# Optimization experiments

Measured on AMD Instinct MI355X. Metric: run time of the kernel, lower is better.

## Reference

```python
import jax, jax.numpy as jnp
import numpy as np

HEAD_NUM = 16
NEG_BIG = -2.0**32 + 1.0


def _pos_encoding(T, D):
    pos = np.arange(T)[:, None].astype(np.float64)
    i = np.arange(D)[None, :].astype(np.float64)
    angle = pos / np.power(10000.0, 2.0 * i / D)
    pe = np.empty((T, D), dtype=np.float64)
    pe[:, 0::2] = np.sin(angle[:, 0::2])
    pe[:, 1::2] = np.cos(angle[:, 1::2])
    return jnp.asarray(pe * (D ** 0.5), dtype=jnp.float32)  # scale=True


def setup_inputs() -> dict:
    key = jax.random.key(0)
    ks = jax.random.split(key, 9)
    B, T, D = 32, 512, 1024
    return {
        "queries": jax.random.normal(ks[0], (B, T, D), jnp.float32),
        "keys": jax.random.normal(ks[1], (B, T, D), jnp.float32),
        "query_masks": jax.random.randint(ks[2], (B, 1), 1, T + 1, jnp.int32),
        "key_masks": jax.random.randint(ks[3], (B, 1), 1, T + 1, jnp.int32),
        "W_Query": jax.random.normal(ks[4], (D, D), jnp.float32) * 0.02,
        "W_key": jax.random.normal(ks[5], (D, D), jnp.float32) * 0.02,
        "W_Value": jax.random.normal(ks[6], (D, D), jnp.float32) * 0.02,
        "fw1": jax.random.normal(ks[7], (D, 4 * D), jnp.float32) * 0.02,
        "fw2": jax.random.normal(ks[8], (4 * D, D), jnp.float32) * 0.02,
    }


def reference(queries, keys, query_masks, key_masks, W_Query, W_key, W_Value, fw1, fw2):
    B, T, D = queries.shape
    h = HEAD_NUM
    d = D // h
    pe = _pos_encoding(T, D)  # [T, D]

    # faithful to source: queries get PE; keys = PE(queries_with_PE) (keys input unused)
    q_pe = queries + pe[None]
    k_pe = q_pe + pe[None]

    qs = jnp.einsum('btd,de->bte', q_pe, W_Query)
    ks_ = jnp.einsum('btd,de->bte', k_pe, W_key)
    vs = jnp.einsum('btd,de->bte', ks_, W_Value)  # faithful: values from projected keys

    def split_heads(x):  # [B,T,h*d] -> [h,B,T,d] (matches tf.split/concat on axis 0)
        return x.reshape(B, T, h, d).transpose(2, 0, 1, 3)

    q4, k4, v4 = split_heads(qs), split_heads(ks_), split_heads(vs)

    scores = jnp.einsum('hbqd,hbkd->hbqk', q4, k4) / (d ** 0.5)

    pos = jnp.arange(T)
    km = (pos[None, :] < key_masks).astype(jnp.float32)    # [B,T]
    qm = (pos[None, :] < query_masks).astype(jnp.float32)  # [B,T]

    scores = jnp.where(km[None, :, None, :] == 1.0, scores, NEG_BIG)
    scores = scores - jnp.max(scores, axis=-1, keepdims=True)
    attn = jax.nn.softmax(scores, axis=-1)
    attn = attn * qm[None, :, :, None]

    out = jnp.einsum('hbqk,hbkd->hbqd', attn, v4)
    result = out.transpose(1, 2, 0, 3).reshape(B, T, D)  # merge heads (head-major)

    result = result + q_pe  # use_res
    # feed forward (use_layer_norm=False, no dropout at inference)
    hmid = jax.nn.relu(jnp.einsum('btd,df->btf', result, fw1))
    result = result + jnp.einsum('btf,fd->btd', hmid, fw2)

    # output_type == 'mean'
    return jnp.mean(result, axis=1, keepdims=True)  # [B,1,D]
```

## Files before the change

kernel.cpp:

```cpp
#include <hip/hip_runtime.h>

constexpr int B_  = 32;
constexpr int T_  = 512;
constexpr int D_  = 1024;
constexpr int NH_ = 16;
constexpr int DH_ = 64;
constexpr int F_  = 4096;
constexpr int BT_ = B_ * T_;

typedef __attribute__((ext_vector_type(8))) short bf16x8;
typedef __attribute__((ext_vector_type(4))) float f32x4;

#define DEVI __device__ __forceinline__

DEVI unsigned short f2bf(float f) {
  union { float f; unsigned u; } uf; uf.f = f;
  unsigned r = uf.u + 0x7fffu + ((uf.u >> 16) & 1u);
  return (unsigned short)(r >> 16);
}
DEVI float b2f(unsigned short h) {
  union { unsigned u; float f; } uf; uf.u = ((unsigned)h) << 16;
  return uf.f;
}
DEVI void gload16(const void* g, void* l) {
  __builtin_amdgcn_global_load_lds(
      (const __attribute__((address_space(1))) void*)(uintptr_t)g,
      (__attribute__((address_space(3))) void*)(unsigned)(uintptr_t)l, 16, 0, 0);
}

__global__ void pe_kernel(float* __restrict__ pe) {
  int idx = blockIdx.x * 256 + threadIdx.x;
  int t = idx >> 10, j = idx & 1023;
  float inv = exp2f(-(2.0f * (float)j / 1024.0f) * 13.2877123795494f);
  float ang = (float)t * inv;
  float v = (j & 1) ? cosf(ang) : sinf(ang);
  pe[idx] = v * 32.0f;
}

__global__ void pack_kernel(const float* __restrict__ q, const float* __restrict__ pe,
                            unsigned short* __restrict__ q_pe, unsigned short* __restrict__ k_pe) {
  long i = ((long)blockIdx.x * 256 + threadIdx.x) * 4;
  const float4 qv = *(const float4*)(q + i);
  const float4 pv = *(const float4*)(pe + (i & (long)(T_ * D_ - 1)));
  ushort4 a, b;
  a.x = f2bf(qv.x + pv.x); a.y = f2bf(qv.y + pv.y);
  a.z = f2bf(qv.z + pv.z); a.w = f2bf(qv.w + pv.w);
  b.x = f2bf(qv.x + 2.f * pv.x); b.y = f2bf(qv.y + 2.f * pv.y);
  b.z = f2bf(qv.z + 2.f * pv.z); b.w = f2bf(qv.w + 2.f * pv.w);
  *(ushort4*)(q_pe + i) = a;
  *(ushort4*)(k_pe + i) = b;
}

__global__ void transpose_w(const float* __restrict__ W, unsigned short* __restrict__ Wt,
                            int K, int N) {
  __shared__ float tile[32][33];
  int tx = threadIdx.x & 31, ty = threadIdx.x >> 5;
  int bx = blockIdx.x, by = blockIdx.y;
  for (int i = 0; i < 4; i++) {
    int r = by * 32 + ty + i * 8;
    tile[ty + i * 8][tx] = W[(long)r * N + bx * 32 + tx];
  }
  __syncthreads();
  for (int i = 0; i < 4; i++) {
    int r = bx * 32 + ty + i * 8;
    Wt[(long)r * K + by * 32 + tx] = f2bf(tile[tx][ty + i * 8]);
  }
}

__global__ void cast_bf16(const float* __restrict__ W, unsigned short* __restrict__ Wb) {
  long i = ((long)blockIdx.x * 256 + threadIdx.x) * 4;
  const float4 v = *(const float4*)(W + i);
  ushort4 o;
  o.x = f2bf(v.x); o.y = f2bf(v.y); o.z = f2bf(v.z); o.w = f2bf(v.w);
  *(ushort4*)(Wb + i) = o;
}

__global__ void transpose_v(const unsigned short* __restrict__ vs, unsigned short* __restrict__ vt) {
  __shared__ unsigned short tile[64][65];
  int bh = blockIdx.y;
  int t0 = blockIdx.x * 64;
  int b = bh >> 4, h = bh & 15;
  int tx = threadIdx.x & 63, ty = threadIdx.x >> 6;
  for (int i = 0; i < 16; i++) {
    int r = i * 4 + ty;
    tile[r][tx] = vs[(long)(b * T_ + t0 + r) * D_ + h * DH_ + tx];
  }
  __syncthreads();
  for (int i = 0; i < 16; i++) {
    int j = i * 4 + ty;
    vt[((long)bh * DH_ + j) * T_ + t0 + tx] = tile[tx][j];
  }
}

template <int EPI>
__global__ __launch_bounds__(256) void gemm_bt(
    const unsigned short* __restrict__ A0, const unsigned short* __restrict__ Bt0,
    unsigned short* __restrict__ C0, float* __restrict__ hacc, int M, int N, int K) {
  __shared__ unsigned short As[128 * 32];
  __shared__ unsigned short Bs[128 * 32];
  const unsigned short* A  = A0;
  const unsigned short* Bt = Bt0;
  unsigned short* C        = C0;

  const int tid = threadIdx.x;
  const int lane = tid & 63, w = tid >> 6;
  const int wr = w >> 1, wc = w & 1;
  const int l15 = lane & 15, lhi = lane >> 4;
  const int brow = blockIdx.y * 128, bcol = blockIdx.x * 128;

  f32x4 acc[4][4] = {};
  const int o = tid * 16;
  const int srow = o >> 6;
  const int skel = (o & 63) >> 1;

  for (int kk = 0; kk < K; kk += 32) {
    gload16(A + (long)(brow + srow) * K + kk + skel,        (char*)As + o);
    gload16(A + (long)(brow + srow + 64) * K + kk + skel,   (char*)As + o + 4096);
    gload16(Bt + (long)(bcol + srow) * K + kk + skel,       (char*)Bs + o);
    gload16(Bt + (long)(bcol + srow + 64) * K + kk + skel,  (char*)Bs + o + 4096);
    __syncthreads();
    bf16x8 af[4], bfr[4];
    for (int m = 0; m < 4; m++)
      af[m] = *(const bf16x8*)((const char*)As + ((wr * 64 + m * 16 + l15) * 64 + lhi * 16));
    for (int n = 0; n < 4; n++)
      bfr[n] = *(const bf16x8*)((const char*)Bs + ((wc * 64 + n * 16 + l15) * 64 + lhi * 16));
    for (int m = 0; m < 4; m++)
      for (int n = 0; n < 4; n++)
        acc[m][n] = __builtin_amdgcn_mfma_f32_16x16x32_bf16(af[m], bfr[n], acc[m][n], 0, 0, 0);
    __syncthreads();
  }

  for (int m = 0; m < 4; m++)
    for (int n = 0; n < 4; n++) {
      int row = brow + wr * 64 + m * 16 + lhi * 4;
      int col = bcol + wc * 64 + n * 16 + l15;
      for (int r = 0; r < 4; r++)
        C[(long)(row + r) * N + col] = f2bf(acc[m][n][r]);
    }
}

template <int EPI>
__global__ __launch_bounds__(512, 2) void gemm8(
    const unsigned short* __restrict__ A0, const unsigned short* __restrict__ Bt0, unsigned short* __restrict__ C0,
    const unsigned short* __restrict__ A1, const unsigned short* __restrict__ Bt1, unsigned short* __restrict__ C1,
    const unsigned short* __restrict__ A2, const unsigned short* __restrict__ Bt2, unsigned short* __restrict__ C2,
    float* __restrict__ hacc, int N,
    const int* __restrict__ L0, const int* __restrict__ L1, const int* __restrict__ L2) {
  constexpr int K = 1024, NK = 16, NI = 8;
  __shared__ char lds[2][2][32768];

  const int z = blockIdx.z;
  const unsigned short* A  = (z == 0) ? A0  : (z == 1 ? A1  : A2);
  const unsigned short* Bt = (z == 0) ? Bt0 : (z == 1 ? Bt1 : Bt2);
  unsigned short* C        = (z == 0) ? C0  : (z == 1 ? C1  : C2);
  const int* L             = (z == 0) ? L0  : (z == 1 ? L1  : L2);

  const long brow = (long)blockIdx.x * 256, bcol = (long)blockIdx.y * 256;
  if (L && (brow & 256) && L[brow >> 9] <= 256) return;

  const int tid = threadIdx.x;
  const int lane = tid & 63, w = tid >> 6;
  const int wm = w >> 2, wn = w & 3;
  const int l15 = lane & 15, lhi = lane >> 4;

  const int drow = (tid * 16) >> 7;
  const int dcol = ((tid * 16) & 127) ^ ((drow & 7) << 4);
  const int sw   = (l15 & 7) << 4;

  f32x4 acc[8][4] = {};
  bf16x8 bfr[4][2], af[2][2];

  auto STAGE = [&](const unsigned short* __restrict__ P, long tb, int kt, int h, int buf, int op) {
    const unsigned short* g = P + (tb + h * 128 + drow) * (long)K + kt * 64 + (dcol >> 1);
    char* l = &lds[buf][op][h * 16384 + tid * 16];
    gload16(g, l);
    gload16(g + 64L * K, l + 8192);
  };
  auto LDA = [&](int buf, int q) {
#pragma unroll
    for (int mi = 0; mi < 2; mi++) {
      int row = wm * 128 + (q * 2 + mi) * 16 + l15;
#pragma unroll
      for (int kk = 0; kk < 2; kk++)
        af[mi][kk] = *(const bf16x8*)(&lds[buf][0][0] + (row << 7) + ((kk * 64 + lhi * 16) ^ sw));
    }
  };
  auto LDB = [&](int buf) {
#pragma unroll
    for (int n = 0; n < 4; n++) {
      int row = wn * 64 + n * 16 + l15;
#pragma unroll
      for (int kk = 0; kk < 2; kk++)
        bfr[n][kk] = *(const bf16x8*)(&lds[buf][1][0] + (row << 7) + ((kk * 64 + lhi * 16) ^ sw));
    }
  };
  auto MFMAQ = [&](int q) {
    __builtin_amdgcn_s_setprio(1);
#pragma unroll
    for (int mi = 0; mi < 2; mi++)
#pragma unroll
      for (int n = 0; n < 4; n++)
#pragma unroll
        for (int kk = 0; kk < 2; kk++)
          acc[q * 2 + mi][n] =
              __builtin_amdgcn_mfma_f32_16x16x32_bf16(af[mi][kk], bfr[n][kk], acc[q * 2 + mi][n], 0, 0, 0);
    __builtin_amdgcn_s_setprio(0);
  };
#define BAR() __builtin_amdgcn_s_barrier()
#define GATE4() asm volatile("s_waitcnt vmcnt(4)" ::: "memory")

  STAGE(A, brow, 0, 0, 0, 0);  STAGE(A, brow, 0, 1, 0, 0);
  STAGE(Bt, bcol, 0, 0, 0, 1); STAGE(Bt, bcol, 0, 1, 0, 1);
  STAGE(Bt, bcol, 1, 0, 1, 1); STAGE(Bt, bcol, 1, 1, 1, 1);
  GATE4();
  BAR();

  for (int i = 0; i < NI; ++i) {
    const int k1 = 2 * i + 1;
    const int ka = (2 * i + 2) & (NK - 1);
    const int kb = (2 * i + 3) & (NK - 1);
    LDA(0, 0); LDB(0); STAGE(A, brow, k1, 0, 1, 0);
    BAR(); MFMAQ(0); BAR();
    LDA(0, 1);         STAGE(A, brow, k1, 1, 1, 0);
    BAR(); MFMAQ(1); BAR();
    LDA(0, 2);         STAGE(Bt, bcol, ka, 0, 0, 1);
    BAR(); MFMAQ(2); BAR();
    LDA(0, 3);         STAGE(Bt, bcol, ka, 1, 0, 1);
    BAR(); MFMAQ(3);
    GATE4();
    BAR();
    LDA(1, 0); LDB(1); STAGE(A, brow, ka, 0, 0, 0);
    BAR(); MFMAQ(0); BAR();
    LDA(1, 1);         STAGE(A, brow, ka, 1, 0, 0);
    BAR(); MFMAQ(1); BAR();
    LDA(1, 2);         STAGE(Bt, bcol, kb, 0, 1, 1);
    BAR(); MFMAQ(2); BAR();
    LDA(1, 3);         STAGE(Bt, bcol, kb, 1, 1, 1);
    BAR(); MFMAQ(3);
    GATE4();
    BAR();
  }
#undef BAR
#undef GATE4

  if (EPI == 0) {
#pragma unroll
    for (int m = 0; m < 8; m++)
#pragma unroll
      for (int n = 0; n < 4; n++) {
        long row = brow + wm * 128 + m * 16 + lhi * 4;
        long col = bcol + wn * 64 + n * 16 + l15;
#pragma unroll
        for (int r = 0; r < 4; r++)
          C[(row + r) * (long)N + col] = f2bf(acc[m][n][r]);
      }
  } else {
    const int batch = (int)(brow >> 9);
#pragma unroll
    for (int n = 0; n < 4; n++) {
      float t = 0.f;
#pragma unroll
      for (int m = 0; m < 8; m++)
#pragma unroll
        for (int r = 0; r < 4; r++) t += fmaxf(acc[m][n][r], 0.f);
      t += __shfl_xor(t, 16);
      t += __shfl_xor(t, 32);
      if (lane < 16)
        atomicAdd(hacc + (long)batch * F_ + bcol + wn * 64 + n * 16 + l15, t);
    }
  }
}

__global__ __launch_bounds__(256, 3) void attn_kernel(
    const unsigned short* __restrict__ qs, const unsigned short* __restrict__ ks,
    const unsigned short* __restrict__ vt, const unsigned short* __restrict__ q_pe,
    const int* __restrict__ qmask, const int* __restrict__ kmask,
    unsigned short* __restrict__ res, float* __restrict__ racc) {
  __shared__ unsigned short Ks[2][64 * 64];
  __shared__ unsigned short Vs[2][64 * 64];
  __shared__ unsigned short Ps[4][32 * 64];

  const int tid = threadIdx.x, lane = tid & 63, w = tid >> 6;
  const int l15 = lane & 15, lhi = lane >> 4;
  const int h = blockIdx.x, b = blockIdx.y, q0 = blockIdx.z * 128;
  const int qlen = qmask[b], kvlen = kmask[b];

  if (q0 >= qlen) {
    int cc = tid & 63;
    float s = 0.f;
    for (int i = 0; i < 32; i++) {
      int r = (tid >> 6) * 32 + i;
      long addr = (long)(b * T_ + q0 + r) * D_ + h * DH_ + cc;
      unsigned short v = q_pe[addr];
      res[addr] = v;
      s += b2f(v);
    }
    atomicAdd(racc + b * D_ + h * DH_ + cc, s);
    return;
  }

  bf16x8 qf[2][2];
  for (int m = 0; m < 2; m++)
    for (int k2 = 0; k2 < 2; k2++) {
      int t = q0 + w * 32 + m * 16 + l15;
      qf[m][k2] = *(const bf16x8*)(qs + (long)(b * T_ + t) * D_ + h * DH_ + k2 * 32 + lhi * 8);
    }

  f32x4 o[2][4] = {};
  float mrun[2][4], lrun[2][4];
  for (int m = 0; m < 2; m++)
    for (int r = 0; r < 4; r++) { mrun[m][r] = -3e38f; lrun[m][r] = 0.f; }

  const float SCL = 0.125f * 1.4426950408889634f;
  const int nc = (kvlen + 63) >> 6;

  auto stage = [&](int c, int buf) {
#pragma unroll
    for (int cl = 0; cl < 2; cl++) {
      int ob = cl * 4096 + tid * 16;
      int os = ob ^ (((ob >> 7) & 7) << 4);
      int r0 = os >> 7, cb = os & 127;
      gload16(ks + (long)(b * T_ + c * 64 + r0) * D_ + h * DH_ + (cb >> 1),
              (char*)&Ks[buf][0] + ob);
      gload16(vt + ((long)(b * NH_ + h) * DH_ + r0) * T_ + c * 64 + (cb >> 1),
              (char*)&Vs[buf][0] + ob);
    }
  };

  stage(0, 0);
  int cur = 0;
  for (int c = 0; c < nc; c++) {
    const int nxt = (c + 1 < nc) ? c + 1 : c;
    stage(nxt, cur ^ 1);
    asm volatile("s_waitcnt vmcnt(4)" ::: "memory");
    __builtin_amdgcn_sched_barrier(0);
    __builtin_amdgcn_s_barrier();

    f32x4 s[2][4] = {};
    for (int k2 = 0; k2 < 2; k2++)
      for (int n = 0; n < 4; n++) {
        int key = n * 16 + l15;
        int Ab = key * 128 + (k2 * 32 + lhi * 8) * 2;
        bf16x8 kf = *(const bf16x8*)((const char*)&Ks[cur][0] + (Ab ^ ((key & 7) << 4)));
        s[0][n] = __builtin_amdgcn_mfma_f32_16x16x32_bf16(qf[0][k2], kf, s[0][n], 0, 0, 0);
        s[1][n] = __builtin_amdgcn_mfma_f32_16x16x32_bf16(qf[1][k2], kf, s[1][n], 0, 0, 0);
      }

    if (c == nc - 1) {
      for (int n = 0; n < 4; n++)
        if (c * 64 + n * 16 + l15 >= kvlen)
          for (int m = 0; m < 2; m++) s[m][n] = f32x4{-3e38f, -3e38f, -3e38f, -3e38f};
    }

    for (int m = 0; m < 2; m++) {
      float mx[4];
      for (int r = 0; r < 4; r++) {
        float v = s[m][0][r];
        for (int n = 1; n < 4; n++) v = fmaxf(v, s[m][n][r]);
        mx[r] = v;
      }
      for (int msk = 1; msk < 16; msk <<= 1)
        for (int r = 0; r < 4; r++) mx[r] = fmaxf(mx[r], __shfl_xor(mx[r], msk));
      float corr[4];
      for (int r = 0; r < 4; r++) {
        float mn = fmaxf(mrun[m][r], mx[r]);
        corr[r] = exp2f((mrun[m][r] - mn) * SCL);
        mrun[m][r] = mn;
      }
      for (int nd = 0; nd < 4; nd++)
        for (int r = 0; r < 4; r++) o[m][nd][r] *= corr[r];
      float ps[4] = {0.f, 0.f, 0.f, 0.f};
      for (int n = 0; n < 4; n++)
        for (int r = 0; r < 4; r++) {
          float pval = exp2f((s[m][n][r] - mrun[m][r]) * SCL);
          s[m][n][r] = pval;
          ps[r] += pval;
        }
      for (int msk = 1; msk < 16; msk <<= 1)
        for (int r = 0; r < 4; r++) ps[r] += __shfl_xor(ps[r], msk);
      for (int r = 0; r < 4; r++) lrun[m][r] = lrun[m][r] * corr[r] + ps[r];
      for (int n = 0; n < 4; n++)
        for (int r = 0; r < 4; r++) {
          int row = m * 16 + lhi * 4 + r;
          int Ab = row * 128 + (n * 16 + l15) * 2;
          *(unsigned short*)((char*)&Ps[w][0] + (Ab ^ ((row & 7) << 4))) = f2bf(s[m][n][r]);
        }
    }
    asm volatile("" ::: "memory");

    for (int k4 = 0; k4 < 2; k4++) {
      bf16x8 pa[2];
      for (int m = 0; m < 2; m++) {
        int row = m * 16 + l15;
        int Ab = row * 128 + k4 * 64 + lhi * 16;
        pa[m] = *(const bf16x8*)((const char*)&Ps[w][0] + (Ab ^ ((row & 7) << 4)));
      }
      for (int nd = 0; nd < 4; nd++) {
        int dv = nd * 16 + l15;
        int Ab = dv * 128 + k4 * 64 + lhi * 16;
        bf16x8 vb = *(const bf16x8*)((const char*)&Vs[cur][0] + (Ab ^ ((dv & 7) << 4)));
        for (int m = 0; m < 2; m++)
          o[m][nd] = __builtin_amdgcn_mfma_f32_16x16x32_bf16(pa[m], vb, o[m][nd], 0, 0, 0);
      }
    }
    __builtin_amdgcn_s_barrier();
    cur ^= 1;
  }

  float cs[4] = {0.f, 0.f, 0.f, 0.f};
  for (int m = 0; m < 2; m++)
    for (int r = 0; r < 4; r++) {
      int t = q0 + w * 32 + m * 16 + lhi * 4 + r;
      float inv = 1.0f / lrun[m][r];
      bool valid = t < qlen;
      for (int nd = 0; nd < 4; nd++) {
        long addr = (long)(b * T_ + t) * D_ + h * DH_ + nd * 16 + l15;
        float v = valid ? o[m][nd][r] * inv : 0.f;
        float val = v + b2f(q_pe[addr]);
        res[addr] = f2bf(val);
        cs[nd] += val;
      }
    }
  for (int nd = 0; nd < 4; nd++) {
    cs[nd] += __shfl_xor(cs[nd], 16);
    cs[nd] += __shfl_xor(cs[nd], 32);
  }
  if (lane < 16)
    for (int nd = 0; nd < 4; nd++)
      atomicAdd(racc + b * D_ + h * DH_ + nd * 16 + l15, cs[nd]);
}

__global__ void initout_kernel(const float* __restrict__ racc, float* __restrict__ out) {
  int i = blockIdx.x * 256 + threadIdx.x;
  out[i] = racc[i] * (1.0f / 512.0f);
}

__global__ void final_kernel(const float* __restrict__ hacc, const float* __restrict__ fw2,
                             float* __restrict__ out) {
  int n = blockIdx.x * 64 + (threadIdx.x & 63);
  int bg = threadIdx.x >> 6;
  int f0 = blockIdx.y * 512;
  float acc[8] = {};
  for (int f = f0; f < f0 + 512; f++) {
    float wv = fw2[(long)f * D_ + n];
    for (int i = 0; i < 8; i++) acc[i] += hacc[(long)(bg * 8 + i) * F_ + f] * wv;
  }
  for (int i = 0; i < 8; i++)
    atomicAdd(out + (bg * 8 + i) * D_ + n, acc[i] * (1.0f / 512.0f));
}

extern "C" void kernel_launch(void* const* d_in, const int* in_sizes, int n_in,
                              void* d_out, int out_size, void* d_ws, size_t ws_size,
                              hipStream_t stream) {
  const float* queries = (const float*)d_in[0];
  const int*   qmask = (const int*)d_in[2];
  const int*   kmask = (const int*)d_in[3];
  const float* Wq  = (const float*)d_in[4];
  const float* Wk  = (const float*)d_in[5];
  const float* Wv  = (const float*)d_in[6];
  const float* fw1 = (const float*)d_in[7];
  const float* fw2 = (const float*)d_in[8];
  float* out = (float*)d_out;

  char* p = (char*)d_ws;
  auto alloc = [&](size_t bytes) -> char* {
    char* r = p; p += (bytes + 255) & ~(size_t)255; return r;
  };
  float*          pe   = (float*)alloc((size_t)T_ * D_ * 4);
  unsigned short* q_pe = (unsigned short*)alloc((size_t)BT_ * D_ * 2);
  unsigned short* k_pe = (unsigned short*)alloc((size_t)BT_ * D_ * 2);
  unsigned short* qs   = (unsigned short*)alloc((size_t)BT_ * D_ * 2);
  unsigned short* ksb  = (unsigned short*)alloc((size_t)BT_ * D_ * 2);
  unsigned short* vt   = (unsigned short*)alloc((size_t)BT_ * D_ * 2);
  unsigned short* res  = (unsigned short*)alloc((size_t)BT_ * D_ * 2);
  unsigned short* Wqt  = (unsigned short*)alloc((size_t)D_ * D_ * 2);
  unsigned short* Wkt  = (unsigned short*)alloc((size_t)D_ * D_ * 2);
  unsigned short* Wvt  = (unsigned short*)alloc((size_t)D_ * D_ * 2);
  unsigned short* Wkbf = (unsigned short*)alloc((size_t)D_ * D_ * 2);
  unsigned short* Wkvt = (unsigned short*)alloc((size_t)D_ * D_ * 2);
  unsigned short* fw1t = (unsigned short*)alloc((size_t)D_ * F_ * 2);
  float*          racc = (float*)alloc((size_t)B_ * D_ * 4);
  float*          hacc = (float*)alloc((size_t)B_ * F_ * 4);
  unsigned short* vs = res;

  hipMemsetAsync(hacc, 0, (size_t)B_ * F_ * 4, stream);
  hipMemsetAsync(racc, 0, (size_t)B_ * D_ * 4, stream);

  pe_kernel<<<T_ * D_ / 256, 256, 0, stream>>>(pe);
  pack_kernel<<<BT_ * D_ / 1024, 256, 0, stream>>>(queries, pe, q_pe, k_pe);
  transpose_w<<<dim3(32, 32), 256, 0, stream>>>(Wq, Wqt, D_, D_);
  transpose_w<<<dim3(32, 32), 256, 0, stream>>>(Wk, Wkt, D_, D_);
  transpose_w<<<dim3(32, 32), 256, 0, stream>>>(Wv, Wvt, D_, D_);
  transpose_w<<<dim3(F_ / 32, 32), 256, 0, stream>>>(fw1, fw1t, D_, F_);
  cast_bf16<<<(D_ * D_) / 1024, 256, 0, stream>>>(Wk, Wkbf);

  gemm_bt<0><<<dim3(8, 8, 1), 256, 0, stream>>>(Wvt, Wkbf, Wkvt, nullptr, D_, D_, D_);

  gemm8<0><<<dim3(64, 4, 3), 512, 0, stream>>>(q_pe, Wqt, qs,
                                               k_pe, Wkt, ksb,
                                               k_pe, Wkvt, vs,
                                               nullptr, D_, qmask, kmask, kmask);

  transpose_v<<<dim3(8, 512), 256, 0, stream>>>(vs, vt);

  attn_kernel<<<dim3(16, 32, 4), 256, 0, stream>>>(qs, ksb, vt, q_pe, qmask, kmask, res, racc);

  gemm8<1><<<dim3(64, 16, 1), 512, 0, stream>>>(res, fw1t, nullptr,
                                                res, fw1t, nullptr,
                                                res, fw1t, nullptr,
                                                hacc, F_, nullptr, nullptr, nullptr);

  initout_kernel<<<(B_ * D_) / 256, 256, 0, stream>>>(racc, out);
  final_kernel<<<dim3(16, 8), 256, 0, stream>>>(hacc, fw2, out);
}
```

Measured before the change: 433.9 us.

## Fuse V transpose into GEMM epilogue and halve barrier phases in main loop

```diff
diff --git a/kernel.cpp b/kernel.cpp
--- a/kernel.cpp
+++ b/kernel.cpp
@@ -73,23 +73,6 @@
   ushort4 o;
   o.x = f2bf(v.x); o.y = f2bf(v.y); o.z = f2bf(v.z); o.w = f2bf(v.w);
   *(ushort4*)(Wb + i) = o;
-}
-
-__global__ void transpose_v(const unsigned short* __restrict__ vs, unsigned short* __restrict__ vt) {
-  __shared__ unsigned short tile[64][65];
-  int bh = blockIdx.y;
-  int t0 = blockIdx.x * 64;
-  int b = bh >> 4, h = bh & 15;
-  int tx = threadIdx.x & 63, ty = threadIdx.x >> 6;
-  for (int i = 0; i < 16; i++) {
-    int r = i * 4 + ty;
-    tile[r][tx] = vs[(long)(b * T_ + t0 + r) * D_ + h * DH_ + tx];
-  }
-  __syncthreads();
-  for (int i = 0; i < 16; i++) {
-    int j = i * 4 + ty;
-    vt[((long)bh * DH_ + j) * T_ + t0 + tx] = tile[tx][j];
-  }
 }
 
 template <int EPI>
@@ -168,7 +151,7 @@
   const int sw   = (l15 & 7) << 4;
 
   f32x4 acc[8][4] = {};
-  bf16x8 bfr[4][2], af[2][2];
+  bf16x8 af[4][2], bfr[4][2];
 
   auto STAGE = [&](const unsigned short* __restrict__ P, long tb, int kt, int h, int buf, int op) {
     const unsigned short* g = P + (tb + h * 128 + drow) * (long)K + kt * 64 + (dcol >> 1);
@@ -176,13 +159,13 @@
     gload16(g, l);
     gload16(g + 64L * K, l + 8192);
   };
-  auto LDA = [&](int buf, int q) {
-#pragma unroll
-    for (int mi = 0; mi < 2; mi++) {
-      int row = wm * 128 + (q * 2 + mi) * 16 + l15;
+  auto LDA4 = [&](int buf, int half) {
+#pragma unroll
+    for (int j = 0; j < 4; j++) {
+      int row = wm * 128 + (half * 4 + j) * 16 + l15;
 #pragma unroll
       for (int kk = 0; kk < 2; kk++)
-        af[mi][kk] = *(const bf16x8*)(&lds[buf][0][0] + (row << 7) + ((kk * 64 + lhi * 16) ^ sw));
+        af[j][kk] = *(const bf16x8*)(&lds[buf][0][0] + (row << 7) + ((kk * 64 + lhi * 16) ^ sw));
     }
   };
   auto LDB = [&](int buf) {
@@ -194,16 +177,16 @@
         bfr[n][kk] = *(const bf16x8*)(&lds[buf][1][0] + (row << 7) + ((kk * 64 + lhi * 16) ^ sw));
     }
   };
-  auto MFMAQ = [&](int q) {
+  auto MFMA4 = [&](int half) {
     __builtin_amdgcn_s_setprio(1);
 #pragma unroll
-    for (int mi = 0; mi < 2; mi++)
+    for (int j = 0; j < 4; j++)
 #pragma unroll
       for (int n = 0; n < 4; n++)
 #pragma unroll
         for (int kk = 0; kk < 2; kk++)
-          acc[q * 2 + mi][n] =
-              __builtin_amdgcn_mfma_f32_16x16x32_bf16(af[mi][kk], bfr[n][kk], acc[q * 2 + mi][n], 0, 0, 0);
+          acc[half * 4 + j][n] =
+              __builtin_amdgcn_mfma_f32_16x16x32_bf16(af[j][kk], bfr[n][kk], acc[half * 4 + j][n], 0, 0, 0);
     __builtin_amdgcn_s_setprio(0);
   };
 #define BAR() __builtin_amdgcn_s_barrier()
@@ -219,24 +202,16 @@
     const int k1 = 2 * i + 1;
     const int ka = (2 * i + 2) & (NK - 1);
     const int kb = (2 * i + 3) & (NK - 1);
-    LDA(0, 0); LDB(0); STAGE(A, brow, k1, 0, 1, 0);
-    BAR(); MFMAQ(0); BAR();
-    LDA(0, 1);         STAGE(A, brow, k1, 1, 1, 0);
-    BAR(); MFMAQ(1); BAR();
-    LDA(0, 2);         STAGE(Bt, bcol, ka, 0, 0, 1);
-    BAR(); MFMAQ(2); BAR();
-    LDA(0, 3);         STAGE(Bt, bcol, ka, 1, 0, 1);
-    BAR(); MFMAQ(3);
+    LDA4(0, 0); LDB(0); STAGE(A, brow, k1, 0, 1, 0); STAGE(A, brow, k1, 1, 1, 0);
+    BAR(); MFMA4(0); BAR();
+    LDA4(0, 1);         STAGE(Bt, bcol, ka, 0, 0, 1); STAGE(Bt, bcol, ka, 1, 0, 1);
+    BAR(); MFMA4(1);
     GATE4();
     BAR();
-    LDA(1, 0); LDB(1); STAGE(A, brow, ka, 0, 0, 0);
-    BAR(); MFMAQ(0); BAR();
-    LDA(1, 1);         STAGE(A, brow, ka, 1, 0, 0);
-    BAR(); MFMAQ(1); BAR();
-    LDA(1, 2);         STAGE(Bt, bcol, kb, 0, 1, 1);
-    BAR(); MFMAQ(2); BAR();
-    LDA(1, 3);         STAGE(Bt, bcol, kb, 1, 1, 1);
-    BAR(); MFMAQ(3);
+    LDA4(1, 0); LDB(1); STAGE(A, brow, ka, 0, 0, 0); STAGE(A, brow, ka, 1, 0, 0);
+    BAR(); MFMA4(0); BAR();
+    LDA4(1, 1);         STAGE(Bt, bcol, kb, 0, 1, 1); STAGE(Bt, bcol, kb, 1, 1, 1);
+    BAR(); MFMA4(1);
     GATE4();
     BAR();
   }
@@ -244,16 +219,34 @@
 #undef GATE4
 
   if (EPI == 0) {
-#pragma unroll
-    for (int m = 0; m < 8; m++)
-#pragma unroll
-      for (int n = 0; n < 4; n++) {
-        long row = brow + wm * 128 + m * 16 + lhi * 4;
-        long col = bcol + wn * 64 + n * 16 + l15;
-#pragma unroll
-        for (int r = 0; r < 4; r++)
-          C[(row + r) * (long)N + col] = f2bf(acc[m][n][r]);
-      }
+    if (z == 2) {
+      const int b  = (int)(brow >> 9);
+      const int t0 = (int)(brow & 511);
+#pragma unroll
+      for (int m = 0; m < 8; m++)
+#pragma unroll
+        for (int n = 0; n < 4; n++) {
+          int col = (int)bcol + wn * 64 + n * 16 + l15;
+          int h = col >> 6, j = col & 63;
+          long vtrow = ((long)(b * NH_ + h)) * DH_ + j;
+          int tl = t0 + wm * 128 + m * 16 + lhi * 4;
+          ushort4 pk;
+          pk.x = f2bf(acc[m][n][0]); pk.y = f2bf(acc[m][n][1]);
+          pk.z = f2bf(acc[m][n][2]); pk.w = f2bf(acc[m][n][3]);
+          *(ushort4*)(C + vtrow * T_ + tl) = pk;
+        }
+    } else {
+#pragma unroll
+      for (int m = 0; m < 8; m++)
+#pragma unroll
+        for (int n = 0; n < 4; n++) {
+          long row = brow + wm * 128 + m * 16 + lhi * 4;
+          long col = bcol + wn * 64 + n * 16 + l15;
+#pragma unroll
+          for (int r = 0; r < 4; r++)
+            C[(row + r) * (long)N + col] = f2bf(acc[m][n][r]);
+        }
+    }
   } else {
     const int batch = (int)(brow >> 9);
 #pragma unroll
@@ -481,7 +474,6 @@
   unsigned short* fw1t = (unsigned short*)alloc((size_t)D_ * F_ * 2);
   float*          racc = (float*)alloc((size_t)B_ * D_ * 4);
   float*          hacc = (float*)alloc((size_t)B_ * F_ * 4);
-  unsigned short* vs = res;
 
   hipMemsetAsync(hacc, 0, (size_t)B_ * F_ * 4, stream);
   hipMemsetAsync(racc, 0, (size_t)B_ * D_ * 4, stream);
@@ -498,10 +490,8 @@
 
   gemm8<0><<<dim3(64, 4, 3), 512, 0, stream>>>(q_pe, Wqt, qs,
                                                k_pe, Wkt, ksb,
-                                               k_pe, Wkvt, vs,
+                                               k_pe, Wkvt, vt,
                                                nullptr, D_, qmask, kmask, kmask);
-
-  transpose_v<<<dim3(8, 512), 256, 0, stream>>>(vs, vt);
 
   attn_kernel<<<dim3(16, 32, 4), 256, 0, stream>>>(qs, ksb, vt, q_pe, qmask, kmask, res, racc);
 
```

Result: no change. 431.0 us (-0.6%).

## Fuse V transpose into GEMM epilogue, lazy softmax rescale, fold output init

Applied to the files above, without the earlier changes.

```diff
diff --git a/kernel.cpp b/kernel.cpp
--- a/kernel.cpp
+++ b/kernel.cpp
@@ -73,23 +73,6 @@
   ushort4 o;
   o.x = f2bf(v.x); o.y = f2bf(v.y); o.z = f2bf(v.z); o.w = f2bf(v.w);
   *(ushort4*)(Wb + i) = o;
-}
-
-__global__ void transpose_v(const unsigned short* __restrict__ vs, unsigned short* __restrict__ vt) {
-  __shared__ unsigned short tile[64][65];
-  int bh = blockIdx.y;
-  int t0 = blockIdx.x * 64;
-  int b = bh >> 4, h = bh & 15;
-  int tx = threadIdx.x & 63, ty = threadIdx.x >> 6;
-  for (int i = 0; i < 16; i++) {
-    int r = i * 4 + ty;
-    tile[r][tx] = vs[(long)(b * T_ + t0 + r) * D_ + h * DH_ + tx];
-  }
-  __syncthreads();
-  for (int i = 0; i < 16; i++) {
-    int j = i * 4 + ty;
-    vt[((long)bh * DH_ + j) * T_ + t0 + tx] = tile[tx][j];
-  }
 }
 
 template <int EPI>
@@ -244,16 +227,41 @@
 #undef GATE4
 
   if (EPI == 0) {
-#pragma unroll
-    for (int m = 0; m < 8; m++)
-#pragma unroll
-      for (int n = 0; n < 4; n++) {
-        long row = brow + wm * 128 + m * 16 + lhi * 4;
-        long col = bcol + wn * 64 + n * 16 + l15;
-#pragma unroll
-        for (int r = 0; r < 4; r++)
-          C[(row + r) * (long)N + col] = f2bf(acc[m][n][r]);
-      }
+    if (z == 2) {
+      char* tl = &lds[0][0][0] + (w << 14);
+#pragma unroll
+      for (int m = 0; m < 8; m++)
+#pragma unroll
+        for (int n = 0; n < 4; n++) {
+          int cl = n * 16 + l15;
+#pragma unroll
+          for (int r = 0; r < 4; r++) {
+            int tofs = m * 16 + lhi * 4 + r;
+            *(unsigned short*)(tl + cl * 256 + ((tofs * 2) ^ ((cl & 7) << 4))) = f2bf(acc[m][n][r]);
+          }
+        }
+      asm volatile("" ::: "memory");
+      const int bb = (int)(brow >> 9), t0 = (int)(brow & 511);
+#pragma unroll
+      for (int rr = 0; rr < 16; rr++) {
+        int row = rr * 4 + lhi;
+        bf16x8 v = *(const bf16x8*)(tl + row * 256 + ((l15 * 16) ^ ((row & 7) << 4)));
+        int gcol = (int)bcol + wn * 64 + row;
+        long vtrow = ((long)(bb * NH_ + (gcol >> 6))) * DH_ + (gcol & 63);
+        *(bf16x8*)(C + vtrow * T_ + t0 + wm * 128 + l15 * 8) = v;
+      }
+    } else {
+#pragma unroll
+      for (int m = 0; m < 8; m++)
+#pragma unroll
+        for (int n = 0; n < 4; n++) {
+          long row = brow + wm * 128 + m * 16 + lhi * 4;
+          long col = bcol + wn * 64 + n * 16 + l15;
+#pragma unroll
+          for (int r = 0; r < 4; r++)
+            C[(row + r) * (long)N + col] = f2bf(acc[m][n][r]);
+        }
+    }
   } else {
     const int batch = (int)(brow >> 9);
 #pragma unroll
@@ -312,6 +320,7 @@
     for (int r = 0; r < 4; r++) { mrun[m][r] = -3e38f; lrun[m][r] = 0.f; }
 
   const float SCL = 0.125f * 1.4426950408889634f;
+  const float THR = 8.0f / SCL;
   const int nc = (kvlen + 63) >> 6;
 
   auto stage = [&](int c, int buf) {
@@ -361,14 +370,19 @@
       }
       for (int msk = 1; msk < 16; msk <<= 1)
         for (int r = 0; r < 4; r++) mx[r] = fmaxf(mx[r], __shfl_xor(mx[r], msk));
-      float corr[4];
-      for (int r = 0; r < 4; r++) {
-        float mn = fmaxf(mrun[m][r], mx[r]);
-        corr[r] = exp2f((mrun[m][r] - mn) * SCL);
-        mrun[m][r] = mn;
-      }
-      for (int nd = 0; nd < 4; nd++)
-        for (int r = 0; r < 4; r++) o[m][nd][r] *= corr[r];
+      bool grow = false;
+      for (int r = 0; r < 4; r++) grow = grow || (mx[r] > mrun[m][r] + THR);
+      if (__any(grow)) {
+        float corr[4];
+        for (int r = 0; r < 4; r++) {
+          float mn = fmaxf(mrun[m][r], mx[r]);
+          corr[r] = exp2f((mrun[m][r] - mn) * SCL);
+          mrun[m][r] = mn;
+        }
+        for (int nd = 0; nd < 4; nd++)
+          for (int r = 0; r < 4; r++) o[m][nd][r] *= corr[r];
+        for (int r = 0; r < 4; r++) lrun[m][r] *= corr[r];
+      }
       float ps[4] = {0.f, 0.f, 0.f, 0.f};
       for (int n = 0; n < 4; n++)
         for (int r = 0; r < 4; r++) {
@@ -378,7 +392,7 @@
         }
       for (int msk = 1; msk < 16; msk <<= 1)
         for (int r = 0; r < 4; r++) ps[r] += __shfl_xor(ps[r], msk);
-      for (int r = 0; r < 4; r++) lrun[m][r] = lrun[m][r] * corr[r] + ps[r];
+      for (int r = 0; r < 4; r++) lrun[m][r] += ps[r];
       for (int n = 0; n < 4; n++)
         for (int r = 0; r < 4; r++) {
           int row = m * 16 + lhi * 4 + r;
@@ -430,13 +444,8 @@
       atomicAdd(racc + b * D_ + h * DH_ + nd * 16 + l15, cs[nd]);
 }
 
-__global__ void initout_kernel(const float* __restrict__ racc, float* __restrict__ out) {
-  int i = blockIdx.x * 256 + threadIdx.x;
-  out[i] = racc[i] * (1.0f / 512.0f);
-}
-
 __global__ void final_kernel(const float* __restrict__ hacc, const float* __restrict__ fw2,
-                             float* __restrict__ out) {
+                             const float* __restrict__ racc, float* __restrict__ out) {
   int n = blockIdx.x * 64 + (threadIdx.x & 63);
   int bg = threadIdx.x >> 6;
   int f0 = blockIdx.y * 512;
@@ -445,6 +454,8 @@
     float wv = fw2[(long)f * D_ + n];
     for (int i = 0; i < 8; i++) acc[i] += hacc[(long)(bg * 8 + i) * F_ + f] * wv;
   }
+  if (blockIdx.y == 0)
+    for (int i = 0; i < 8; i++) acc[i] += racc[(long)(bg * 8 + i) * D_ + n];
   for (int i = 0; i < 8; i++)
     atomicAdd(out + (bg * 8 + i) * D_ + n, acc[i] * (1.0f / 512.0f));
 }
@@ -481,10 +492,10 @@
   unsigned short* fw1t = (unsigned short*)alloc((size_t)D_ * F_ * 2);
   float*          racc = (float*)alloc((size_t)B_ * D_ * 4);
   float*          hacc = (float*)alloc((size_t)B_ * F_ * 4);
-  unsigned short* vs = res;
 
   hipMemsetAsync(hacc, 0, (size_t)B_ * F_ * 4, stream);
   hipMemsetAsync(racc, 0, (size_t)B_ * D_ * 4, stream);
+  hipMemsetAsync(out, 0, (size_t)B_ * D_ * 4, stream);
 
   pe_kernel<<<T_ * D_ / 256, 256, 0, stream>>>(pe);
   pack_kernel<<<BT_ * D_ / 1024, 256, 0, stream>>>(queries, pe, q_pe, k_pe);
@@ -498,10 +509,8 @@
 
   gemm8<0><<<dim3(64, 4, 3), 512, 0, stream>>>(q_pe, Wqt, qs,
                                                k_pe, Wkt, ksb,
-                                               k_pe, Wkvt, vs,
+                                               k_pe, Wkvt, vt,
                                                nullptr, D_, qmask, kmask, kmask);
-
-  transpose_v<<<dim3(8, 512), 256, 0, stream>>>(vs, vt);
 
   attn_kernel<<<dim3(16, 32, 4), 256, 0, stream>>>(qs, ksb, vt, q_pe, qmask, kmask, res, racc);
 
@@ -510,6 +519,5 @@
                                                 res, fw1t, nullptr,
                                                 hacc, F_, nullptr, nullptr, nullptr);
 
-  initout_kernel<<<(B_ * D_) / 256, 256, 0, stream>>>(racc, out);
-  final_kernel<<<dim3(16, 8), 256, 0, stream>>>(hacc, fw2, out);
-}
+  final_kernel<<<dim3(16, 8), 256, 0, stream>>>(hacc, fw2, racc, out);
+}
```

Measured after the change: 416.1 us. -4.1%, faster.
